# Performance work log

Measured on AMD Instinct MI355X. Metric: run time of the kernel, lower is better.

The kernel has to match this reference:

```python
import jax, jax.numpy as jnp
import numpy as np

B, T, IN, OUT = 32, 2048, 1024, 256
DT = 1.0
TAU_MIN, TAU_MAX = 15.0, 25.0


def setup_inputs() -> dict:
    key = jax.random.key(0)
    k1, k2, k3 = jax.random.split(key, 3)
    inputs = jax.random.normal(k1, (B, T, IN), dtype=jnp.float32)
    bound = float(np.sqrt(1.0 / IN))
    weight = jax.random.uniform(k2, (OUT, IN), minval=-bound, maxval=bound, dtype=jnp.float32)
    bias = jnp.zeros((OUT,), dtype=jnp.float32)
    tau = jax.random.uniform(k3, (OUT,), minval=TAU_MIN, maxval=TAU_MAX, dtype=jnp.float32)
    decay = jnp.exp(-DT / tau)  # per-channel leak alpha in (0,1)
    return {"inputs": inputs, "weight": weight, "bias": bias, "decay": decay}


def reference(inputs, weight, bias, decay):
    # Dense projection: [B,T,IN] @ [IN,OUT] -> [B,T,OUT]
    current = jnp.einsum("bti,oi->bto", inputs, weight) + bias
    # Leaky integrator: u_t = alpha * u_{t-1} + (1-alpha) * x_t, u_0 = 0
    one_minus = 1.0 - decay

    def step(u, x):  # u,x: [B,OUT]
        u = decay * u + one_minus * x
        return u, u

    u0 = jnp.zeros((inputs.shape[0], weight.shape[0]), dtype=current.dtype)
    _, us = jax.lax.scan(step, u0, jnp.swapaxes(current, 0, 1))  # [T,B,OUT]
    return jnp.swapaxes(us, 0, 1)  # [B,T,OUT]
```

## Files before the change

### kernel.cpp

```cpp
#include <hip/hip_runtime.h>

#define B_   32
#define T_   2048
#define IN_  1024
#define OUT_ 256
#define M_   (B_ * T_)

#define BM 128
#define BN 256
#define BK 32
#define NSTEPS (IN_ / BK)
#define THREADS 512

#define LC 32
#define NC (T_ / LC)
#define XPAD 264

#define ABUF_OFF(c) ((c) * (BM * BK * 2))
#define BBUF_OFF(c) (3 * (BM * BK * 2) + (c) * (BN * BK * 2))
#define SMEM_BYTES (3 * (BM * BK * 2) + 3 * (BN * BK * 2))

typedef __attribute__((ext_vector_type(4))) float f32x4;
typedef __attribute__((ext_vector_type(8))) __bf16 bf16x8;

__device__ __forceinline__ unsigned int f2bf_pk(float a, float b) {
    unsigned int ua = __float_as_uint(a);
    unsigned int ub = __float_as_uint(b);
    ua = (ua + 0x7fffu + ((ua >> 16) & 1u)) >> 16;
    ub = (ub + 0x7fffu + ((ub >> 16) & 1u)) >> 16;
    return ua | (ub << 16);
}
__device__ __forceinline__ unsigned short f2bf1(float a) {
    unsigned int ua = __float_as_uint(a);
    return (unsigned short)((ua + 0x7fffu + ((ua >> 16) & 1u)) >> 16);
}
__device__ __forceinline__ float bf2f(unsigned short s) {
    return __uint_as_float((unsigned int)s << 16);
}

__device__ __forceinline__ void gload_lds16(const void* g, void* l) {
    __builtin_amdgcn_global_load_lds(
        (const __attribute__((address_space(1))) void*)g,
        (__attribute__((address_space(3))) void*)l, 16, 0, 0);
}

__global__ __launch_bounds__(256) void convert_w(const float* __restrict__ W,
                                                 unsigned short* __restrict__ Wb) {
    const int i = blockIdx.x * 256 + threadIdx.x;
    const float4 v = ((const float4*)W)[i];
    uint2 o;
    o.x = f2bf_pk(v.x, v.y);
    o.y = f2bf_pk(v.z, v.w);
    ((uint2*)Wb)[i] = o;
}

__global__ __launch_bounds__(THREADS, 4) void gemm_fused(
    const float* __restrict__ A, const unsigned short* __restrict__ Wb,
    const float* __restrict__ bias, const float* __restrict__ decay,
    unsigned short* __restrict__ Xb, float* __restrict__ chunkend) {
    __shared__ __align__(16) char smem[SMEM_BYTES];

    const int tid  = threadIdx.x;
    const int lane = tid & 63;
    const int wid  = tid >> 6;
    const int wm   = wid >> 2;
    const int wn   = wid & 3;
    const int l15  = lane & 15;
    const int l4   = lane >> 4;
    const int bm0  = blockIdx.x * BM;

    const int rowA = tid >> 2;
    const int gA   = tid & 3;
    const float* gsrcA = A + (size_t)(bm0 + rowA) * IN_ + gA * 8;
    const int ldsA = rowA * BK + ((gA ^ (rowA & 3)) << 3);

    const unsigned short* gsrcB[2];
    int ldsBbase[2];
#pragma unroll
    for (int i = 0; i < 2; ++i) {
        const int q = (wid + i * 8) * 64 + lane;
        const int r = q >> 2;
        const int g = (q & 3) ^ (r & 3);
        gsrcB[i] = Wb + (size_t)r * IN_ + g * 8;
        ldsBbase[i] = (wid + i * 8) * 1024;
    }

    f32x4 acc[4][4] = {};
    float4 a0, a1;

    gload_lds16(gsrcB[0], smem + BBUF_OFF(0) + ldsBbase[0]);
    gload_lds16(gsrcB[1], smem + BBUF_OFF(0) + ldsBbase[1]);
    a0 = *(const float4*)(gsrcA);
    a1 = *(const float4*)(gsrcA + 4);
    {
        int4 w;
        w.x = f2bf_pk(a0.x, a0.y); w.y = f2bf_pk(a0.z, a0.w);
        w.z = f2bf_pk(a1.x, a1.y); w.w = f2bf_pk(a1.z, a1.w);
        *(int4*)(smem + ABUF_OFF(0) + ldsA * 2) = w;
    }
    a0 = *(const float4*)(gsrcA + BK);
    a1 = *(const float4*)(gsrcA + BK + 4);
    asm volatile("s_waitcnt lgkmcnt(0)" ::: "memory");
    __builtin_amdgcn_s_barrier();
    __builtin_amdgcn_sched_barrier(0);
    gload_lds16(gsrcB[0] + BK, smem + BBUF_OFF(1) + ldsBbase[0]);
    gload_lds16(gsrcB[1] + BK, smem + BBUF_OFF(1) + ldsBbase[1]);

    for (int i = 0; i < NSTEPS; ++i) {
        if (i + 1 < NSTEPS) {
            asm volatile("s_waitcnt vmcnt(2)" ::: "memory");
        } else {
            asm volatile("s_waitcnt vmcnt(0)" ::: "memory");
        }
        __builtin_amdgcn_sched_barrier(0);
        if (i + 1 < NSTEPS) {
            int4 w;
            w.x = f2bf_pk(a0.x, a0.y); w.y = f2bf_pk(a0.z, a0.w);
            w.z = f2bf_pk(a1.x, a1.y); w.w = f2bf_pk(a1.z, a1.w);
            *(int4*)(smem + ABUF_OFF((i + 1) % 3) + ldsA * 2) = w;
        }
        if (i + 2 < NSTEPS) {
            const int k0 = (i + 2) * BK;
            a0 = *(const float4*)(gsrcA + k0);
            a1 = *(const float4*)(gsrcA + k0 + 4);
        }
        asm volatile("s_waitcnt lgkmcnt(0)" ::: "memory");
        __builtin_amdgcn_s_barrier();
        __builtin_amdgcn_sched_barrier(0);
        if (i + 2 < NSTEPS) {
            const int k0 = (i + 2) * BK;
            gload_lds16(gsrcB[0] + k0, smem + BBUF_OFF((i + 2) % 3) + ldsBbase[0]);
            gload_lds16(gsrcB[1] + k0, smem + BBUF_OFF((i + 2) % 3) + ldsBbase[1]);
        }
        {
            const unsigned short* Ab = (const unsigned short*)(smem + ABUF_OFF(i % 3));
            const unsigned short* Bb = (const unsigned short*)(smem + BBUF_OFF(i % 3));
            bf16x8 af[4], bfv[4];
#pragma unroll
            for (int mi = 0; mi < 4; ++mi) {
                const int row = wm * 64 + mi * 16 + l15;
                af[mi] = *(const bf16x8*)&Ab[row * BK + ((l4 ^ (row & 3)) << 3)];
            }
#pragma unroll
            for (int ni = 0; ni < 4; ++ni) {
                const int col = wn * 64 + ni * 16 + l15;
                bfv[ni] = *(const bf16x8*)&Bb[col * BK + ((l4 ^ (col & 3)) << 3)];
            }
#pragma unroll
            for (int mi = 0; mi < 4; ++mi)
#pragma unroll
                for (int ni = 0; ni < 4; ++ni)
                    acc[mi][ni] = __builtin_amdgcn_mfma_f32_16x16x32_bf16(
                        af[mi], bfv[ni], acc[mi][ni], 0, 0, 0);
        }
    }
    __syncthreads();

    unsigned short* xt = (unsigned short*)smem;
#pragma unroll
    for (int ni = 0; ni < 4; ++ni) {
        const int col = wn * 64 + ni * 16 + l15;
        const float bv = bias[col];
#pragma unroll
        for (int mi = 0; mi < 4; ++mi) {
            const int r0 = wm * 64 + mi * 16 + (l4 << 2);
#pragma unroll
            for (int r = 0; r < 4; ++r)
                xt[(r0 + r) * XPAD + col] = f2bf1(acc[mi][ni][r] + bv);
        }
    }
    __syncthreads();

    const int b  = bm0 >> 11;
    const int c0 = (bm0 >> 5) & 63;

    {
        const int cr = tid >> 5;
        const int cg = (tid & 31) << 3;
#pragma unroll
        for (int it = 0; it < 8; ++it) {
            const int row = it * 16 + cr;
            bf16x8 v = *(const bf16x8*)&xt[row * XPAD + cg];
            *(bf16x8*)&Xb[(size_t)(bm0 + row) * OUT_ + cg] = v;
        }
    }

    for (int task = tid; task < 4 * OUT_; task += THREADS) {
        const int cl  = task >> 8;
        const int col = task & 255;
        const float alpha = decay[col];
        const float om = 1.0f - alpha;
        float u = 0.0f;
        const unsigned short* p = &xt[(cl * LC) * XPAD + col];
#pragma unroll
        for (int t = 0; t < LC; ++t)
            u = fmaf(alpha, u, om * bf2f(p[t * XPAD]));
        chunkend[(size_t)(b * NC + c0 + cl) * OUT_ + col] = u;
    }
}

__global__ __launch_bounds__(OUT_) void carry_pass(const float* __restrict__ chunkend,
                                                   const float* __restrict__ decay,
                                                   float* __restrict__ carryin) {
    const int b = blockIdx.x;
    const int o = threadIdx.x;
    const float alpha = decay[o];
    float aL = alpha;
#pragma unroll
    for (int i = 1; i < LC; ++i) aL *= alpha;

    float ce[NC];
#pragma unroll
    for (int c = 0; c < NC; ++c)
        ce[c] = chunkend[(size_t)(b * NC + c) * OUT_ + o];

    float carry = 0.0f;
#pragma unroll
    for (int c = 0; c < NC; ++c) {
        carryin[(size_t)(b * NC + c) * OUT_ + o] = carry;
        carry = fmaf(aL, carry, ce[c]);
    }
}

__global__ __launch_bounds__(256) void scan_final(const unsigned short* __restrict__ Xb,
                                                  const float* __restrict__ decay,
                                                  const float* __restrict__ carryin,
                                                  float* __restrict__ out) {
    const int unit = blockIdx.x * 4 + (threadIdx.x >> 6);
    const int l    = threadIdx.x & 63;
    const int col  = l << 2;
    const int b    = unit >> 6;
    const int c    = unit & 63;

    const float4 al = *(const float4*)&decay[col];
    const float4 om = {1.0f - al.x, 1.0f - al.y, 1.0f - al.z, 1.0f - al.w};
    float4 u = *(const float4*)&carryin[(size_t)unit * OUT_ + col];

    const size_t base = (size_t)(b * T_ + c * LC) * OUT_ + col;
#pragma unroll 8
    for (int t = 0; t < LC; ++t) {
        const ushort4 xv = *(const ushort4*)&Xb[base + (size_t)t * OUT_];
        u.x = fmaf(al.x, u.x, om.x * bf2f(xv.x));
        u.y = fmaf(al.y, u.y, om.y * bf2f(xv.y));
        u.z = fmaf(al.z, u.z, om.z * bf2f(xv.z));
        u.w = fmaf(al.w, u.w, om.w * bf2f(xv.w));
        *(float4*)&out[base + (size_t)t * OUT_] = u;
    }
}

__global__ __launch_bounds__(256) void gemm_bias(const float* __restrict__ A,
                                                 const float* __restrict__ W,
                                                 const float* __restrict__ bias,
                                                 float* __restrict__ C) {
    __shared__ float As[16][64 + 4];
    __shared__ float Ws[16][64 + 4];
    const int bm = blockIdx.y * 64;
    const int bn = blockIdx.x * 64;
    const int tid = threadIdx.x;
    const int tx = tid & 15, ty = tid >> 4;
    const int lr = tid >> 2, lc = (tid & 3) << 2;
    float acc[4][4] = {};
    const float* Ap = A + (size_t)(bm + lr) * IN_ + lc;
    const float* Wp = W + (size_t)(bn + lr) * IN_ + lc;
    for (int k0 = 0; k0 < IN_; k0 += 16) {
        const float4 a = *(const float4*)(Ap + k0);
        const float4 w = *(const float4*)(Wp + k0);
        __syncthreads();
        As[lc + 0][lr] = a.x; As[lc + 1][lr] = a.y; As[lc + 2][lr] = a.z; As[lc + 3][lr] = a.w;
        Ws[lc + 0][lr] = w.x; Ws[lc + 1][lr] = w.y; Ws[lc + 2][lr] = w.z; Ws[lc + 3][lr] = w.w;
        __syncthreads();
#pragma unroll
        for (int kk = 0; kk < 16; ++kk) {
            const float4 av = *(const float4*)&As[kk][ty << 2];
            const float4 wv = *(const float4*)&Ws[kk][tx << 2];
            const float a0[4] = {av.x, av.y, av.z, av.w};
            const float w0[4] = {wv.x, wv.y, wv.z, wv.w};
#pragma unroll
            for (int i = 0; i < 4; ++i)
#pragma unroll
                for (int j = 0; j < 4; ++j) acc[i][j] = fmaf(a0[i], w0[j], acc[i][j]);
        }
    }
#pragma unroll
    for (int i = 0; i < 4; ++i) {
        const size_t row = (size_t)(bm + (ty << 2) + i);
#pragma unroll
        for (int j = 0; j < 4; ++j)
            C[row * OUT_ + bn + (tx << 2) + j] = acc[i][j] + bias[bn + (tx << 2) + j];
    }
}

__global__ __launch_bounds__(OUT_) void scan_simple(float* __restrict__ C,
                                                    const float* __restrict__ decay) {
    const int b = blockIdx.x;
    const int o = threadIdx.x;
    const float alpha = decay[o];
    const float om = 1.0f - alpha;
    float u = 0.0f;
    float* p = C + (size_t)b * T_ * OUT_ + o;
    for (int t = 0; t < T_; ++t) {
        const float x = p[(size_t)t * OUT_];
        u = fmaf(alpha, u, om * x);
        p[(size_t)t * OUT_] = u;
    }
}

extern "C" void kernel_launch(void* const* d_in, const int* in_sizes, int n_in,
                              void* d_out, int out_size, void* d_ws, size_t ws_size,
                              hipStream_t stream) {
    const float* inputs = (const float*)d_in[0];
    const float* weight = (const float*)d_in[1];
    const float* bias   = (const float*)d_in[2];
    const float* decay  = (const float*)d_in[3];
    float* out = (float*)d_out;

    const size_t wb_bytes = (size_t)OUT_ * IN_ * 2;
    const size_t ce_bytes = (size_t)B_ * NC * OUT_ * 4;
    const size_t ci_bytes = ce_bytes;
    const size_t x_bytes  = (size_t)M_ * OUT_ * 2;
    const size_t need = wb_bytes + ce_bytes + ci_bytes + x_bytes;

    if (ws_size >= need) {
        char* w = (char*)d_ws;
        unsigned short* Wb = (unsigned short*)w;
        float* chunkend    = (float*)(w + wb_bytes);
        float* carryin     = (float*)(w + wb_bytes + ce_bytes);
        unsigned short* Xb = (unsigned short*)(w + wb_bytes + ce_bytes + ci_bytes);

        convert_w<<<(OUT_ * IN_ / 4) / 256, 256, 0, stream>>>(weight, Wb);
        gemm_fused<<<M_ / BM, THREADS, 0, stream>>>(inputs, Wb, bias, decay, Xb, chunkend);
        carry_pass<<<B_, OUT_, 0, stream>>>(chunkend, decay, carryin);
        scan_final<<<(B_ * NC) / 4, 256, 0, stream>>>(Xb, decay, carryin, out);
    } else {
        dim3 g(OUT_ / 64, M_ / 64);
        gemm_bias<<<g, 256, 0, stream>>>(inputs, weight, bias, out);
        scan_simple<<<B_, OUT_, 0, stream>>>(out, decay);
    }
}
```

Before: 114.9 us.

## Fuse GEMM, carry propagation and final scan into one kernel with tile flags

Merges the carry pass and final scan into the GEMM kernel. Tiles get a dynamic ticket order through an atomic counter and publish per-tile chunk-end states with release flags. Each tile waits on earlier tiles within a group of 16 (one sequence of 2048 steps) to build its carry-in, then writes the fp32 output directly from LDS. This removes the bf16 intermediate round trip to global memory and two kernel launches, at the cost of inter-block spin-waiting and a serial dependency chain within each sequence.

```diff
diff --git a/kernel.cpp b/kernel.cpp
--- a/kernel.cpp
+++ b/kernel.cpp
@@ -11,14 +11,15 @@
 #define BK 32
 #define NSTEPS (IN_ / BK)
 #define THREADS 512
+#define TPB 16
 
 #define LC 32
-#define NC (T_ / LC)
 #define XPAD 264
 
 #define ABUF_OFF(c) ((c) * (BM * BK * 2))
 #define BBUF_OFF(c) (3 * (BM * BK * 2) + (c) * (BN * BK * 2))
-#define SMEM_BYTES (3 * (BM * BK * 2) + 3 * (BN * BK * 2))
+#define XT_BYTES (BM * XPAD * 2)
+#define SMEM_BYTES (XT_BYTES + 8192)
 
 typedef __attribute__((ext_vector_type(4))) float f32x4;
 typedef __attribute__((ext_vector_type(8))) __bf16 bf16x8;
@@ -44,21 +45,29 @@
         (__attribute__((address_space(3))) void*)l, 16, 0, 0);
 }
 
-__global__ __launch_bounds__(256) void convert_w(const float* __restrict__ W,
-                                                 unsigned short* __restrict__ Wb) {
+__global__ __launch_bounds__(256) void convert_w_init(const float* __restrict__ W,
+                                                      unsigned short* __restrict__ Wb,
+                                                      unsigned int* __restrict__ flags) {
     const int i = blockIdx.x * 256 + threadIdx.x;
     const float4 v = ((const float4*)W)[i];
     uint2 o;
     o.x = f2bf_pk(v.x, v.y);
     o.y = f2bf_pk(v.z, v.w);
     ((uint2*)Wb)[i] = o;
-}
-
-__global__ __launch_bounds__(THREADS, 4) void gemm_fused(
+    if (blockIdx.x == 0) {
+        flags[threadIdx.x] = 0u;
+        flags[256 + threadIdx.x] = 0u;
+        if (threadIdx.x == 0) flags[512] = 0u;
+    }
+}
+
+__global__ __launch_bounds__(THREADS, 4) void fused_all(
     const float* __restrict__ A, const unsigned short* __restrict__ Wb,
     const float* __restrict__ bias, const float* __restrict__ decay,
-    unsigned short* __restrict__ Xb, float* __restrict__ chunkend) {
+    float* __restrict__ out, float* __restrict__ localend,
+    unsigned int* __restrict__ flags) {
     __shared__ __align__(16) char smem[SMEM_BYTES];
+    __shared__ int s_tk;
 
     const int tid  = threadIdx.x;
     const int lane = tid & 63;
@@ -67,7 +76,13 @@
     const int wn   = wid & 3;
     const int l15  = lane & 15;
     const int l4   = lane >> 4;
-    const int bm0  = blockIdx.x * BM;
+
+    if (tid == 0) s_tk = (int)atomicAdd(&flags[512], 1u);
+    __syncthreads();
+    const int p    = s_tk;
+    const int jb   = p & (TPB - 1);
+    const int base = p - jb;
+    const int bm0  = p * BM;
 
     const int rowA = tid >> 2;
     const int gA   = tid & 3;
@@ -157,6 +172,9 @@
     __syncthreads();
 
     unsigned short* xt = (unsigned short*)smem;
+    float* ceL = (float*)(smem + XT_BYTES);
+    float* caL = ceL + 4 * OUT_;
+
 #pragma unroll
     for (int ni = 0; ni < 4; ++ni) {
         const int col = wn * 64 + ni * 16 + l15;
@@ -170,20 +188,6 @@
         }
     }
     __syncthreads();
-
-    const int b  = bm0 >> 11;
-    const int c0 = (bm0 >> 5) & 63;
-
-    {
-        const int cr = tid >> 5;
-        const int cg = (tid & 31) << 3;
-#pragma unroll
-        for (int it = 0; it < 8; ++it) {
-            const int row = it * 16 + cr;
-            bf16x8 v = *(const bf16x8*)&xt[row * XPAD + cg];
-            *(bf16x8*)&Xb[(size_t)(bm0 + row) * OUT_ + cg] = v;
-        }
-    }
 
     for (int task = tid; task < 4 * OUT_; task += THREADS) {
         const int cl  = task >> 8;
@@ -191,60 +195,70 @@
         const float alpha = decay[col];
         const float om = 1.0f - alpha;
         float u = 0.0f;
-        const unsigned short* p = &xt[(cl * LC) * XPAD + col];
+        const unsigned short* px = &xt[(cl * LC) * XPAD + col];
 #pragma unroll
         for (int t = 0; t < LC; ++t)
-            u = fmaf(alpha, u, om * bf2f(p[t * XPAD]));
-        chunkend[(size_t)(b * NC + c0 + cl) * OUT_ + col] = u;
-    }
-}
-
-__global__ __launch_bounds__(OUT_) void carry_pass(const float* __restrict__ chunkend,
-                                                   const float* __restrict__ decay,
-                                                   float* __restrict__ carryin) {
-    const int b = blockIdx.x;
-    const int o = threadIdx.x;
-    const float alpha = decay[o];
-    float aL = alpha;
-#pragma unroll
-    for (int i = 1; i < LC; ++i) aL *= alpha;
-
-    float ce[NC];
-#pragma unroll
-    for (int c = 0; c < NC; ++c)
-        ce[c] = chunkend[(size_t)(b * NC + c) * OUT_ + o];
-
-    float carry = 0.0f;
-#pragma unroll
-    for (int c = 0; c < NC; ++c) {
-        carryin[(size_t)(b * NC + c) * OUT_ + o] = carry;
-        carry = fmaf(aL, carry, ce[c]);
-    }
-}
-
-__global__ __launch_bounds__(256) void scan_final(const unsigned short* __restrict__ Xb,
-                                                  const float* __restrict__ decay,
-                                                  const float* __restrict__ carryin,
-                                                  float* __restrict__ out) {
-    const int unit = blockIdx.x * 4 + (threadIdx.x >> 6);
-    const int l    = threadIdx.x & 63;
-    const int col  = l << 2;
-    const int b    = unit >> 6;
-    const int c    = unit & 63;
-
-    const float4 al = *(const float4*)&decay[col];
-    const float4 om = {1.0f - al.x, 1.0f - al.y, 1.0f - al.z, 1.0f - al.w};
-    float4 u = *(const float4*)&carryin[(size_t)unit * OUT_ + col];
-
-    const size_t base = (size_t)(b * T_ + c * LC) * OUT_ + col;
-#pragma unroll 8
-    for (int t = 0; t < LC; ++t) {
-        const ushort4 xv = *(const ushort4*)&Xb[base + (size_t)t * OUT_];
-        u.x = fmaf(al.x, u.x, om.x * bf2f(xv.x));
-        u.y = fmaf(al.y, u.y, om.y * bf2f(xv.y));
-        u.z = fmaf(al.z, u.z, om.z * bf2f(xv.z));
-        u.w = fmaf(al.w, u.w, om.w * bf2f(xv.w));
-        *(float4*)&out[base + (size_t)t * OUT_] = u;
+            u = fmaf(alpha, u, om * bf2f(px[t * XPAD]));
+        ceL[cl * OUT_ + col] = u;
+    }
+    __syncthreads();
+
+    float alpha_c = 0.f, a32 = 0.f, a128 = 0.f;
+    if (tid < OUT_) {
+        alpha_c = decay[tid];
+        a32 = alpha_c;
+#pragma unroll
+        for (int i = 1; i < LC; ++i) a32 *= alpha_c;
+        const float t2 = a32 * a32;
+        a128 = t2 * t2;
+        float le = ceL[tid];
+        le = fmaf(a32, le, ceL[OUT_ + tid]);
+        le = fmaf(a32, le, ceL[2 * OUT_ + tid]);
+        le = fmaf(a32, le, ceL[3 * OUT_ + tid]);
+        __hip_atomic_store(&localend[(size_t)p * OUT_ + tid], le,
+                           __ATOMIC_RELAXED, __HIP_MEMORY_SCOPE_AGENT);
+    }
+    __syncthreads();
+    if (tid == 0)
+        __hip_atomic_store(&flags[p], 1u, __ATOMIC_RELEASE, __HIP_MEMORY_SCOPE_AGENT);
+    if (tid < jb) {
+        while (__hip_atomic_load(&flags[base + tid], __ATOMIC_ACQUIRE,
+                                 __HIP_MEMORY_SCOPE_AGENT) == 0u)
+            __builtin_amdgcn_s_sleep(2);
+    }
+    __syncthreads();
+
+    if (tid < OUT_) {
+        float cin = 0.0f;
+#pragma unroll
+        for (int i = 0; i < TPB - 1; ++i) {
+            float v = __hip_atomic_load(&localend[(size_t)(base + i) * OUT_ + tid],
+                                        __ATOMIC_RELAXED, __HIP_MEMORY_SCOPE_AGENT);
+            if (i < jb) cin = fmaf(a128, cin, v);
+        }
+        caL[tid] = cin;
+        const float c1 = fmaf(a32, cin, ceL[tid]);
+        const float c2 = fmaf(a32, c1, ceL[OUT_ + tid]);
+        const float c3 = fmaf(a32, c2, ceL[2 * OUT_ + tid]);
+        caL[OUT_ + tid] = c1;
+        caL[2 * OUT_ + tid] = c2;
+        caL[3 * OUT_ + tid] = c3;
+    }
+    __syncthreads();
+
+    for (int task = tid; task < 4 * OUT_; task += THREADS) {
+        const int cl  = task >> 8;
+        const int col = task & 255;
+        const float alpha = decay[col];
+        const float om = 1.0f - alpha;
+        float u = caL[cl * OUT_ + col];
+        const unsigned short* px = &xt[(cl * LC) * XPAD + col];
+        float* po = &out[(size_t)(bm0 + cl * LC) * OUT_ + col];
+#pragma unroll
+        for (int t = 0; t < LC; ++t) {
+            u = fmaf(alpha, u, om * bf2f(px[t * XPAD]));
+            po[(size_t)t * OUT_] = u;
+        }
     }
 }
 
@@ -315,22 +329,19 @@
     float* out = (float*)d_out;
 
     const size_t wb_bytes = (size_t)OUT_ * IN_ * 2;
-    const size_t ce_bytes = (size_t)B_ * NC * OUT_ * 4;
-    const size_t ci_bytes = ce_bytes;
-    const size_t x_bytes  = (size_t)M_ * OUT_ * 2;
-    const size_t need = wb_bytes + ce_bytes + ci_bytes + x_bytes;
+    const size_t le_bytes = (size_t)(M_ / BM) * OUT_ * 4;
+    const size_t fl_bytes = 4096;
+    const size_t need = wb_bytes + le_bytes + fl_bytes;
 
     if (ws_size >= need) {
         char* w = (char*)d_ws;
-        unsigned short* Wb = (unsigned short*)w;
-        float* chunkend    = (float*)(w + wb_bytes);
-        float* carryin     = (float*)(w + wb_bytes + ce_bytes);
-        unsigned short* Xb = (unsigned short*)(w + wb_bytes + ce_bytes + ci_bytes);
-
-        convert_w<<<(OUT_ * IN_ / 4) / 256, 256, 0, stream>>>(weight, Wb);
-        gemm_fused<<<M_ / BM, THREADS, 0, stream>>>(inputs, Wb, bias, decay, Xb, chunkend);
-        carry_pass<<<B_, OUT_, 0, stream>>>(chunkend, decay, carryin);
-        scan_final<<<(B_ * NC) / 4, 256, 0, stream>>>(Xb, decay, carryin, out);
+        unsigned short* Wb  = (unsigned short*)w;
+        float* localend     = (float*)(w + wb_bytes);
+        unsigned int* flags = (unsigned int*)(w + wb_bytes + le_bytes);
+
+        convert_w_init<<<(OUT_ * IN_ / 4) / 256, 256, 0, stream>>>(weight, Wb, flags);
+        fused_all<<<M_ / BM, THREADS, 0, stream>>>(inputs, Wb, bias, decay,
+                                                   out, localend, flags);
     } else {
         dim3 g(OUT_ / 64, M_ / 64);
         gemm_bias<<<g, 256, 0, stream>>>(inputs, weight, bias, out);
```

Result: no change. 113.0 us (-1.7%).
